# Kernel optimization log

Measured on AMD Instinct MI355X. Metric: run time of the kernel, lower is better.

The kernel has to match this reference:

```python
import jax, jax.numpy as jnp
import numpy as np

HEADS = 4
ALPHA = 0.2  # leaky relu negative slope


def setup_inputs() -> dict:
    key = jax.random.key(0)
    ks = jax.random.split(key, 8)
    N, Fin, Fout = 4096, 512, 256
    return {
        "h": jax.random.normal(ks[0], (N, Fin), dtype=jnp.float32),
        "adj": jax.random.randint(ks[1], (N, N), 0, 2, dtype=jnp.int32),
        "W": jax.random.normal(ks[2], (Fin, Fout), dtype=jnp.float32) * (Fin ** -0.5),
        "Wl_w": jax.random.normal(ks[3], (Fout, Fout), dtype=jnp.float32) * (Fout ** -0.5),
        "Wl_b": jax.random.normal(ks[4], (Fout,), dtype=jnp.float32) * 0.02,
        "Wqkv_w": jax.random.normal(ks[5], (3 * Fout, Fout), dtype=jnp.float32) * (Fout ** -0.5),
        "Wqkv_b": jax.random.normal(ks[6], (3 * Fout,), dtype=jnp.float32) * 0.02,
        "a": jax.random.normal(ks[7], (2 * Fout, 1), dtype=jnp.float32) * (Fout ** -0.5),
    }


def reference(h, adj, W, Wl_w, Wl_b, Wqkv_w, Wqkv_b, a):
    N = h.shape[0]
    Fout = W.shape[1]
    d = Fout // HEADS
    scale = Fout ** -0.5  # note: original scales by out_features^-0.5, not head_dim

    Wh = h @ W                      # [N, Fout]
    Wh = Wh @ Wl_w.T + Wl_b         # to_linear

    qkv = Wh @ Wqkv_w.T + Wqkv_b    # [N, 3*Fout]
    q, k, v = jnp.split(qkv, 3, axis=-1)
    to_heads = lambda t: t.reshape(N, HEADS, d).transpose(1, 0, 2)  # [H, N, d]
    q, k, v = to_heads(q), to_heads(k), to_heads(v)

    dots = jax.nn.softmax(jnp.einsum('hid,hjd->hij', q, k) * scale, axis=-1)  # [H,N,N]
    Wh0 = jnp.einsum('hij,hjd->hid', dots, v)            # [H, N, d]
    Wh0 = Wh0.transpose(1, 0, 2).reshape(N, Fout)        # i (h d)
    Wh0 = jax.nn.softmax(Wh0, axis=-1)

    # GAT score decomposed: e_ij = leakyrelu(Wh_i . a1 + Wh_j . a2)
    a1 = a[:Fout, 0]
    a2 = a[Fout:, 0]
    e = jax.nn.leaky_relu((Wh @ a1)[:, None] + (Wh @ a2)[None, :], negative_slope=ALPHA)

    dsum = dots.sum(axis=0)                              # [N, N]
    neg = jnp.float32(-9e15)
    attention = jnp.where(adj > 0, e + dsum, neg)
    attention = jax.nn.softmax(attention, axis=1)
    # dropout p=0.0 / eval mode -> identity

    h_prime = attention @ Wh + Wh0
    return jax.nn.elu(h_prime)  # concat=True
```

## Files before the change

kernel.cpp:

```cpp
#include <hip/hip_runtime.h>

typedef float  f32x4 __attribute__((ext_vector_type(4)));
typedef short  s16x8 __attribute__((ext_vector_type(8)));
typedef unsigned short u16x8 __attribute__((ext_vector_type(8)));

#define NROWS 4096
#define ALPHA_LR 0.2f
#define SCALE 0.0625f

static __device__ __forceinline__ unsigned short bf16_rne(float x) {
    unsigned u = __float_as_uint(x);
    u += 0x7fffu + ((u >> 16) & 1u);
    return (unsigned short)(u >> 16);
}
static __device__ __forceinline__ unsigned short bf16_trunc(float x) {
    return (unsigned short)(__float_as_uint(x) >> 16);
}
static __device__ __forceinline__ float bf2f(unsigned short h) {
    return __uint_as_float(((unsigned)h) << 16);
}
static __device__ __forceinline__ float bflo(unsigned u) { return __uint_as_float(u << 16); }
static __device__ __forceinline__ float bfhi(unsigned u) { return __uint_as_float(u & 0xffff0000u); }
static __device__ __forceinline__ float wmax16(float v) {
#pragma unroll
    for (int o = 8; o; o >>= 1) v = fmaxf(v, __shfl_xor(v, o, 16));
    return v;
}
static __device__ __forceinline__ float wsum16(float v) {
#pragma unroll
    for (int o = 8; o; o >>= 1) v += __shfl_xor(v, o, 16);
    return v;
}

__global__ __launch_bounds__(256) void wprep(
    const float* __restrict__ W, const float* __restrict__ Wq,
    unsigned short* __restrict__ Whi, unsigned short* __restrict__ Wlo,
    unsigned short* __restrict__ Qhi, unsigned short* __restrict__ Qlo)
{
    int i = blockIdx.x * 256 + threadIdx.x;
    if (i < 131072) {
        float v = W[i];
        unsigned short hh = bf16_trunc(v);
        Whi[i] = hh; Wlo[i] = bf16_rne(v - bf2f(hh));
    }
    if (i < 196608) {
        float v = Wq[i];
        unsigned short hh = bf16_trunc(v);
        Qhi[i] = hh; Qlo[i] = bf16_rne(v - bf2f(hh));
    }
}

template <int EPI, bool BIAS>
__global__ __launch_bounds__(256) void gemm_mfma(
    const float* __restrict__ A,
    const unsigned short* __restrict__ Bhi, const unsigned short* __restrict__ Blo,
    const float* __restrict__ bias,
    float* __restrict__ C, unsigned short* __restrict__ o0,
    unsigned short* __restrict__ o1, unsigned short* __restrict__ o2,
    int M, int Nn, int K)
{
    __shared__ unsigned short Ah[64][40];
    __shared__ unsigned short Al[64][40];
    __shared__ unsigned short Bh[64][40];
    __shared__ unsigned short Bl[64][40];

    const int tid = threadIdx.x;
    const int w = tid >> 6;
    const int ln = tid & 63;
    const int l15 = ln & 15;
    const int lhi = ln >> 4;
    const int bm = blockIdx.y * 64;
    const int bn = blockIdx.x * 64;
    const int sm = tid >> 2;
    const int sk = (tid & 3) * 8;

    f32x4 acc[4];
#pragma unroll
    for (int cf = 0; cf < 4; ++cf) acc[cf] = (f32x4){0.f, 0.f, 0.f, 0.f};

    const float* arow = &A[(size_t)(bm + sm) * K];
    const unsigned short* bhrow = &Bhi[(size_t)(bn + sm) * K];
    const unsigned short* blrow = &Blo[(size_t)(bn + sm) * K];

    float4 a0r = *(const float4*)(arow + sk);
    float4 a1r = *(const float4*)(arow + sk + 4);
    uint4 bhr = *(const uint4*)(bhrow + sk);
    uint4 blr = *(const uint4*)(blrow + sk);

    for (int k0 = 0; k0 < K; k0 += 32) {
        float vv[8] = {a0r.x, a0r.y, a0r.z, a0r.w, a1r.x, a1r.y, a1r.z, a1r.w};
        unsigned hp[4], lp[4];
#pragma unroll
        for (int q = 0; q < 4; ++q) {
            unsigned short h0 = bf16_trunc(vv[q * 2]);
            unsigned short h1 = bf16_trunc(vv[q * 2 + 1]);
            unsigned short l0 = bf16_rne(vv[q * 2] - bf2f(h0));
            unsigned short l1 = bf16_rne(vv[q * 2 + 1] - bf2f(h1));
            hp[q] = (unsigned)h0 | ((unsigned)h1 << 16);
            lp[q] = (unsigned)l0 | ((unsigned)l1 << 16);
        }
        __syncthreads();
        *(uint4*)&Ah[sm][sk] = make_uint4(hp[0], hp[1], hp[2], hp[3]);
        *(uint4*)&Al[sm][sk] = make_uint4(lp[0], lp[1], lp[2], lp[3]);
        *(uint4*)&Bh[sm][sk] = bhr;
        *(uint4*)&Bl[sm][sk] = blr;
        const int kn = (k0 + 32 < K) ? k0 + 32 : 0;
        a0r = *(const float4*)(arow + kn + sk);
        a1r = *(const float4*)(arow + kn + sk + 4);
        bhr = *(const uint4*)(bhrow + kn + sk);
        blr = *(const uint4*)(blrow + kn + sk);
        __syncthreads();
        s16x8 ah = *(const s16x8*)&Ah[w * 16 + l15][lhi * 8];
        s16x8 al2 = *(const s16x8*)&Al[w * 16 + l15][lhi * 8];
        __builtin_amdgcn_s_setprio(1);
#pragma unroll
        for (int cf = 0; cf < 4; ++cf) {
            s16x8 bh = *(const s16x8*)&Bh[cf * 16 + l15][lhi * 8];
            s16x8 bl = *(const s16x8*)&Bl[cf * 16 + l15][lhi * 8];
            acc[cf] = __builtin_amdgcn_mfma_f32_16x16x32_bf16(ah, bh, acc[cf], 0, 0, 0);
            acc[cf] = __builtin_amdgcn_mfma_f32_16x16x32_bf16(ah, bl, acc[cf], 0, 0, 0);
            acc[cf] = __builtin_amdgcn_mfma_f32_16x16x32_bf16(al2, bh, acc[cf], 0, 0, 0);
        }
        __builtin_amdgcn_s_setprio(0);
    }

#pragma unroll
    for (int cf = 0; cf < 4; ++cf) {
        const int col = bn + cf * 16 + l15;
        float bv = BIAS ? bias[col] : 0.0f;
#pragma unroll
        for (int r = 0; r < 4; ++r) {
            const int row = bm + w * 16 + lhi * 4 + r;
            float v = acc[cf][r] + bv;
            if (EPI == 1) {
                C[(size_t)row * Nn + col] = v;
                o0[(size_t)col * NROWS + row] = bf16_rne(v);
            } else if (EPI == 2) {
                if (col < 256)      o0[(size_t)row * 256 + col] = bf16_rne(v);
                else if (col < 512) o1[(size_t)row * 256 + (col - 256)] = bf16_rne(v);
                else                o2[(size_t)(col - 512) * NROWS + row] = bf16_rne(v);
            } else {
                unsigned short hh = bf16_trunc(v);
                o0[(size_t)row * Nn + col] = hh;
                o1[(size_t)row * Nn + col] = bf16_rne(v - bf2f(hh));
            }
        }
    }
}

__global__ __launch_bounds__(256) void compute_p(
    const float* __restrict__ Wh, const float* __restrict__ a,
    float* __restrict__ p1, float* __restrict__ p2)
{
    const int row = blockIdx.x * 16 + (threadIdx.x >> 4);
    const int c = threadIdx.x & 15;
    float s1 = 0.f, s2 = 0.f;
    for (int f = c; f < 256; f += 16) {
        float w = Wh[(size_t)row * 256 + f];
        s1 += w * a[f];
        s2 += w * a[256 + f];
    }
    s1 = wsum16(s1);
    s2 = wsum16(s2);
    if (c == 0) { p1[row] = s1; p2[row] = s2; }
}

__global__ __launch_bounds__(256) void p2max_kernel(
    const float* __restrict__ p2, float* __restrict__ p2m)
{
    __shared__ float red[4];
    const int tid = threadIdx.x;
    float v = -3.0e38f;
#pragma unroll
    for (int k = 0; k < 16; ++k) v = fmaxf(v, p2[tid + k * 256]);
#pragma unroll
    for (int o = 32; o; o >>= 1) v = fmaxf(v, __shfl_xor(v, o, 64));
    if ((tid & 63) == 0) red[tid >> 6] = v;
    __syncthreads();
    if (tid == 0) p2m[0] = fmaxf(fmaxf(red[0], red[1]), fmaxf(red[2], red[3]));
}

__global__ __launch_bounds__(256) void norms1(
    const unsigned short* __restrict__ qh, const unsigned short* __restrict__ kh,
    float* __restrict__ qn2, float* __restrict__ knp)
{
    __shared__ float kn[16][4];
    const int tid = threadIdx.x;
    const int r16 = tid >> 4;
    const int c = tid & 15;
    const int i = blockIdx.x * 16 + r16;
#pragma unroll
    for (int h = 0; h < 4; ++h) {
        float sq = 0.f, sk = 0.f;
#pragma unroll
        for (int d = 0; d < 4; ++d) {
            float qv = bf2f(qh[(size_t)i * 256 + h * 64 + c + d * 16]);
            float kv = bf2f(kh[(size_t)i * 256 + h * 64 + c + d * 16]);
            sq += qv * qv; sk += kv * kv;
        }
        sq = wsum16(sq); sk = wsum16(sk);
        if (c == 0) { qn2[i * 4 + h] = sq; kn[r16][h] = sk; }
    }
    __syncthreads();
    if (tid < 4) {
        float m = 0.f;
#pragma unroll
        for (int r = 0; r < 16; ++r) m = fmaxf(m, kn[r][tid]);
        knp[blockIdx.x * 4 + tid] = m;
    }
}

__global__ __launch_bounds__(256) void norms2(
    const float* __restrict__ qn2, const float* __restrict__ knp,
    float* __restrict__ Mb)
{
    __shared__ float red[4][4];
    __shared__ float kmax[4];
    const int tid = threadIdx.x;
    float v[4];
#pragma unroll
    for (int h = 0; h < 4; ++h) v[h] = knp[tid * 4 + h];
#pragma unroll
    for (int h = 0; h < 4; ++h)
#pragma unroll
        for (int o = 32; o; o >>= 1) v[h] = fmaxf(v[h], __shfl_xor(v[h], o, 64));
    if ((tid & 63) == 0) {
#pragma unroll
        for (int h = 0; h < 4; ++h) red[tid >> 6][h] = v[h];
    }
    __syncthreads();
    if (tid < 4)
        kmax[tid] = fmaxf(fmaxf(red[0][tid], red[1][tid]), fmaxf(red[2][tid], red[3][tid]));
    __syncthreads();
    const int i = blockIdx.x * 256 + tid;
#pragma unroll
    for (int h = 0; h < 4; ++h)
        Mb[i * 4 + h] = sqrtf(qn2[i * 4 + h] * kmax[h]) * SCALE;
}

__global__ __launch_bounds__(256) void zsum_kernel(
    const unsigned short* __restrict__ qh_g, const unsigned short* __restrict__ kh_g,
    const float* __restrict__ Mb, float* __restrict__ zpart)
{
    const int tid = threadIdx.x;
    const int h = tid >> 6;
    const int ln = tid & 63;
    const int l15 = ln & 15;
    const int lhi = ln >> 4;
    const int rt = blockIdx.x & 255;
    const int ch = blockIdx.x >> 8;
    const int i0 = rt * 16;

    s16x8 qA[2];
#pragma unroll
    for (int ks = 0; ks < 2; ++ks)
        qA[ks] = *(const s16x8*)(qh_g + (size_t)(i0 + l15) * 256 + h * 64 + ks * 32 + lhi * 8);
    float M[4];
#pragma unroll
    for (int r = 0; r < 4; ++r) M[r] = Mb[(i0 + lhi * 4 + r) * 4 + h];

    float z[4] = {0.f, 0.f, 0.f, 0.f};
    s16x8 kfc[2][2];
#pragma unroll
    for (int nt = 0; nt < 2; ++nt)
#pragma unroll
        for (int ks = 0; ks < 2; ++ks)
            kfc[nt][ks] = *(const s16x8*)(kh_g + (size_t)(ch * 1024 + nt * 16 + l15) * 256 +
                                          h * 64 + ks * 32 + lhi * 8);

    for (int tt = 0; tt < 32; ++tt) {
        const int jn = ch * 1024 + ((tt + 1) & 31) * 32;
        f32x4 acc[2] = {{0.f,0.f,0.f,0.f},{0.f,0.f,0.f,0.f}};
        __builtin_amdgcn_s_setprio(1);
#pragma unroll
        for (int ks = 0; ks < 2; ++ks)
#pragma unroll
            for (int nt = 0; nt < 2; ++nt)
                acc[nt] = __builtin_amdgcn_mfma_f32_16x16x32_bf16(qA[ks], kfc[nt][ks], acc[nt], 0, 0, 0);
        __builtin_amdgcn_s_setprio(0);
#pragma unroll
        for (int nt = 0; nt < 2; ++nt)
#pragma unroll
            for (int ks = 0; ks < 2; ++ks)
                kfc[nt][ks] = *(const s16x8*)(kh_g + (size_t)(jn + nt * 16 + l15) * 256 +
                                              h * 64 + ks * 32 + lhi * 8);
#pragma unroll
        for (int r = 0; r < 4; ++r)
            z[r] += __expf(acc[0][r] * SCALE - M[r]) + __expf(acc[1][r] * SCALE - M[r]);
    }
#pragma unroll
    for (int r = 0; r < 4; ++r) {
        float zz = wsum16(z[r]);
        if (l15 == 0)
            zpart[(((size_t)(i0 + lhi * 4 + r) * 4 + h) * 4) + ch] = zz;
    }
}

__global__ __launch_bounds__(256) void pvds_kernel(
    const unsigned short* __restrict__ qh_g, const unsigned short* __restrict__ kh_g,
    const unsigned short* __restrict__ vth_g,
    const float* __restrict__ Mb, const float* __restrict__ zpart,
    unsigned short* __restrict__ dsum_g, unsigned short* __restrict__ pacc_o)
{
    enum { D0 = 0, D1 = 5120, MIZ = 10240, SMEMSZ = 10752 };
    __shared__ __align__(16) char smem[SMEMSZ];

    const int tid = threadIdx.x;
    const int h = tid >> 6;
    const int ln = tid & 63;
    const int l15 = ln & 15;
    const int lhi = ln >> 4;
    const int rt = blockIdx.x & 255;
    const int ch = blockIdx.x >> 8;
    const int i0 = rt * 16;
    const int srow = tid >> 4;
    const int sc2 = (tid & 15) * 2;

    if (tid < 64) {
        int hh = tid >> 4, row = tid & 15;
        float M = Mb[(i0 + row) * 4 + hh];
        const float* zb = zpart + ((size_t)(i0 + row) * 4 + hh) * 4;
        float z = ((zb[0] + zb[1]) + zb[2]) + zb[3];
        float* fl = (float*)(smem + MIZ);
        fl[(hh * 16 + row) * 2] = M;
        fl[(hh * 16 + row) * 2 + 1] = 1.0f / z;
    }

    s16x8 qA[2];
#pragma unroll
    for (int ks = 0; ks < 2; ++ks)
        qA[ks] = *(const s16x8*)(qh_g + (size_t)(i0 + l15) * 256 + h * 64 + ks * 32 + lhi * 8);
    __syncthreads();

    float m_f[4], iz_f[4];
#pragma unroll
    for (int r = 0; r < 4; ++r) {
        m_f[r]  = ((float*)(smem + MIZ))[(h * 16 + lhi * 4 + r) * 2];
        iz_f[r] = ((float*)(smem + MIZ))[(h * 16 + lhi * 4 + r) * 2 + 1];
    }

    s16x8 kfc[2][2], vfc[2];
#pragma unroll
    for (int nt = 0; nt < 2; ++nt)
#pragma unroll
        for (int ks = 0; ks < 2; ++ks)
            kfc[nt][ks] = *(const s16x8*)(kh_g + (size_t)(ch * 1024 + nt * 16 + l15) * 256 +
                                          h * 64 + ks * 32 + lhi * 8);
#pragma unroll
    for (int nt = 0; nt < 2; ++nt)
        vfc[nt] = *(const s16x8*)(vth_g + (size_t)(h * 64 + nt * 16 + l15) * 4096 +
                                  ch * 1024 + lhi * 8);

    f32x4 pacc[2] = {{0.f,0.f,0.f,0.f},{0.f,0.f,0.f,0.f}};

    for (int tt = 0; tt < 32; ++tt) {
        const int j0 = ch * 1024 + tt * 32;
        const int jn = ch * 1024 + ((tt + 1) & 31) * 32;
        const int buf = (tt & 1) ? D1 : D0;

        f32x4 acc[2] = {{0.f,0.f,0.f,0.f},{0.f,0.f,0.f,0.f}};
        __builtin_amdgcn_s_setprio(1);
#pragma unroll
        for (int ks = 0; ks < 2; ++ks)
#pragma unroll
            for (int nt = 0; nt < 2; ++nt)
                acc[nt] = __builtin_amdgcn_mfma_f32_16x16x32_bf16(qA[ks], kfc[nt][ks], acc[nt], 0, 0, 0);
        __builtin_amdgcn_s_setprio(0);
#pragma unroll
        for (int nt = 0; nt < 2; ++nt)
#pragma unroll
            for (int ks = 0; ks < 2; ++ks)
                kfc[nt][ks] = *(const s16x8*)(kh_g + (size_t)(jn + nt * 16 + l15) * 256 +
                                              h * 64 + ks * 32 + lhi * 8);
#pragma unroll
        for (int nt = 0; nt < 2; ++nt)
#pragma unroll
            for (int r = 0; r < 4; ++r) {
                float d = __expf(acc[nt][r] * SCALE - m_f[r]) * iz_f[r];
                int row = lhi * 4 + r;
                *(unsigned short*)(smem + buf + h * 1280 + row * 80 + (nt * 16 + l15) * 2) = bf16_rne(d);
            }
        __syncthreads();

        {
            s16x8 dA = *(const s16x8*)(smem + buf + h * 1280 + l15 * 80 + lhi * 16);
            __builtin_amdgcn_s_setprio(1);
            pacc[0] = __builtin_amdgcn_mfma_f32_16x16x32_bf16(dA, vfc[0], pacc[0], 0, 0, 0);
            pacc[1] = __builtin_amdgcn_mfma_f32_16x16x32_bf16(dA, vfc[1], pacc[1], 0, 0, 0);
            __builtin_amdgcn_s_setprio(0);
        }
#pragma unroll
        for (int nt = 0; nt < 2; ++nt)
            vfc[nt] = *(const s16x8*)(vth_g + (size_t)(h * 64 + nt * 16 + l15) * 4096 + jn + lhi * 8);

        {
            float ds0 = 0.f, ds1 = 0.f;
#pragma unroll
            for (int hh = 0; hh < 4; ++hh) {
                unsigned u = *(const unsigned*)(smem + buf + hh * 1280 + srow * 80 + sc2 * 2);
                ds0 += bflo(u); ds1 += bfhi(u);
            }
            unsigned pk = (unsigned)bf16_rne(ds0) | ((unsigned)bf16_rne(ds1) << 16);
            *(unsigned*)(dsum_g + (size_t)(i0 + srow) * 4096 + j0 + sc2) = pk;
        }
    }

    const size_t pbase = (size_t)(rt * 4 + ch) * 4096;
#pragma unroll
    for (int nt = 0; nt < 2; ++nt)
#pragma unroll
        for (int r = 0; r < 4; ++r)
            pacc_o[pbase + (lhi * 4 + r) * 256 + h * 64 + nt * 16 + l15] = bf16_rne(pacc[nt][r]);
}

__global__ __launch_bounds__(256) void outer_kernel(
    const unsigned short* __restrict__ wht_g, const unsigned short* __restrict__ dsum_g,
    const float* __restrict__ p1g, const float* __restrict__ p2g,
    const float* __restrict__ p2m, const int* __restrict__ adj,
    unsigned short* __restrict__ wacc_o, float* __restrict__ Lp_o)
{
    enum { PT0 = 0, PT1 = 2304, SMEMSZ = 4608 };
    __shared__ __align__(16) char smem[SMEMSZ];

    const int tid = threadIdx.x;
    const int w = tid >> 6;
    const int ln = tid & 63;
    const int l15 = ln & 15;
    const int lhi = ln >> 4;
    const int rt = blockIdx.x & 255;
    const int ch = blockIdx.x >> 8;
    const int i0 = rt * 16;
    const int jbase = ch * 1024;
    const int srow = tid >> 4;
    const int sc4 = (tid & 15) * 4;

    const float p1v = p1g[i0 + srow];
    float Mfix;
    {
        float s = p1v + p2m[0];
        Mfix = (s > 0.f ? s : ALPHA_LR * s) + 4.0f;
    }

    int4   adjc = *(const int4*)(adj + (size_t)(i0 + srow) * 4096 + jbase + sc4);
    ushort4 dsc = *(const ushort4*)(dsum_g + (size_t)(i0 + srow) * 4096 + jbase + sc4);
    float4 p2c  = *(const float4*)(p2g + jbase + sc4);
    s16x8 wfc[4][2];
#pragma unroll
    for (int nt = 0; nt < 4; ++nt)
#pragma unroll
        for (int ks = 0; ks < 2; ++ks)
            wfc[nt][ks] = *(const s16x8*)(wht_g + (size_t)(w * 64 + nt * 16 + l15) * 4096 +
                                          jbase + ks * 32 + lhi * 8);

    f32x4 acc[4];
#pragma unroll
    for (int nt = 0; nt < 4; ++nt) acc[nt] = (f32x4){0.f, 0.f, 0.f, 0.f};
    float Lacc = 0.0f;

    for (int t = 0; t < 16; ++t) {
        const int jn = jbase + ((t + 1) & 15) * 64;
        const int buf = (t & 1) ? PT1 : PT0;

        {
            float pr[4];
            float dsv[4] = {bf2f(dsc.x), bf2f(dsc.y), bf2f(dsc.z), bf2f(dsc.w)};
            float p2v[4] = {p2c.x, p2c.y, p2c.z, p2c.w};
            int   av[4]  = {adjc.x, adjc.y, adjc.z, adjc.w};
#pragma unroll
            for (int k = 0; k < 4; ++k) {
                float e = p1v + p2v[k];
                e = e > 0.f ? e : ALPHA_LR * e;
                pr[k] = (av[k] > 0) ? __expf(e + dsv[k] - Mfix) : 0.f;
                Lacc += pr[k];
            }
            ushort4 pk;
            pk.x = bf16_rne(pr[0]); pk.y = bf16_rne(pr[1]);
            pk.z = bf16_rne(pr[2]); pk.w = bf16_rne(pr[3]);
            *(ushort4*)(smem + buf + srow * 144 + sc4 * 2) = pk;
        }
        adjc = *(const int4*)(adj + (size_t)(i0 + srow) * 4096 + jn + sc4);
        dsc  = *(const ushort4*)(dsum_g + (size_t)(i0 + srow) * 4096 + jn + sc4);
        p2c  = *(const float4*)(p2g + jn + sc4);
        __syncthreads();

        {
            s16x8 pa0 = *(const s16x8*)(smem + buf + l15 * 144 + lhi * 16);
            s16x8 pa1 = *(const s16x8*)(smem + buf + l15 * 144 + 64 + lhi * 16);
            __builtin_amdgcn_s_setprio(1);
#pragma unroll
            for (int nt = 0; nt < 4; ++nt) {
                acc[nt] = __builtin_amdgcn_mfma_f32_16x16x32_bf16(pa0, wfc[nt][0], acc[nt], 0, 0, 0);
                acc[nt] = __builtin_amdgcn_mfma_f32_16x16x32_bf16(pa1, wfc[nt][1], acc[nt], 0, 0, 0);
            }
            __builtin_amdgcn_s_setprio(0);
        }
#pragma unroll
        for (int nt = 0; nt < 4; ++nt)
#pragma unroll
            for (int ks = 0; ks < 2; ++ks)
                wfc[nt][ks] = *(const s16x8*)(wht_g + (size_t)(w * 64 + nt * 16 + l15) * 4096 +
                                              jn + ks * 32 + lhi * 8);
    }

    Lacc = wsum16(Lacc);
    if ((tid & 15) == 0) Lp_o[(size_t)(rt * 4 + ch) * 16 + srow] = Lacc;

    const size_t wbase = (size_t)(rt * 4 + ch) * 4096;
#pragma unroll
    for (int nt = 0; nt < 4; ++nt)
#pragma unroll
        for (int r = 0; r < 4; ++r)
            wacc_o[wbase + (lhi * 4 + r) * 256 + w * 64 + nt * 16 + l15] = bf16_rne(acc[nt][r]);
}

__global__ __launch_bounds__(256) void merge_kernel(
    const unsigned short* __restrict__ pacc_b, const unsigned short* __restrict__ wacc_b,
    const float* __restrict__ Lp, float* __restrict__ out)
{
    const int rt = blockIdx.x;
    const int tid = threadIdx.x;
    const int row = tid >> 4;
    const int cg = tid & 15;

    float L = 0.f;
#pragma unroll
    for (int c = 0; c < 4; ++c) L += Lp[(size_t)(rt * 4 + c) * 16 + row];
    const float invL = 1.0f / fmaxf(L, 1e-30f);

    float p[16], wv[16];
#pragma unroll
    for (int k = 0; k < 16; ++k) { p[k] = 0.f; wv[k] = 0.f; }
#pragma unroll
    for (int c = 0; c < 4; ++c) {
        const size_t b = (size_t)(rt * 4 + c) * 4096 + row * 256 + cg * 16;
        u16x8 pa0 = *(const u16x8*)(pacc_b + b);
        u16x8 pa1 = *(const u16x8*)(pacc_b + b + 8);
        u16x8 wa0 = *(const u16x8*)(wacc_b + b);
        u16x8 wa1 = *(const u16x8*)(wacc_b + b + 8);
#pragma unroll
        for (int k = 0; k < 8; ++k) {
            p[k] += bf2f(pa0[k]);  p[k + 8] += bf2f(pa1[k]);
            wv[k] += bf2f(wa0[k]); wv[k + 8] += bf2f(wa1[k]);
        }
    }

    float mx = -3.0e38f;
#pragma unroll
    for (int k = 0; k < 16; ++k) mx = fmaxf(mx, p[k]);
    mx = wmax16(mx);
    float sm = 0.f;
#pragma unroll
    for (int k = 0; k < 16; ++k) { p[k] = __expf(p[k] - mx); sm += p[k]; }
    sm = wsum16(sm);
    const float inv = 1.0f / sm;

    float* orow = out + ((size_t)(rt * 16 + row)) * 256 + cg * 16;
#pragma unroll
    for (int k4 = 0; k4 < 4; ++k4) {
        float4 o;
        float v;
        v = wv[k4*4+0] * invL + p[k4*4+0] * inv; o.x = v > 0.f ? v : __expf(v) - 1.f;
        v = wv[k4*4+1] * invL + p[k4*4+1] * inv; o.y = v > 0.f ? v : __expf(v) - 1.f;
        v = wv[k4*4+2] * invL + p[k4*4+2] * inv; o.z = v > 0.f ? v : __expf(v) - 1.f;
        v = wv[k4*4+3] * invL + p[k4*4+3] * inv; o.w = v > 0.f ? v : __expf(v) - 1.f;
        *(float4*)(orow + k4 * 4) = o;
    }
}

extern "C" void kernel_launch(void* const* d_in, const int* in_sizes, int n_in,
                              void* d_out, int out_size, void* d_ws, size_t ws_size,
                              hipStream_t stream)
{
    const float* h      = (const float*)d_in[0];
    const int*   adj    = (const int*)d_in[1];
    const float* W      = (const float*)d_in[2];
    const float* Wl_w   = (const float*)d_in[3];
    const float* Wl_b   = (const float*)d_in[4];
    const float* Wqkv_w = (const float*)d_in[5];
    const float* Wqkv_b = (const float*)d_in[6];
    const float* a      = (const float*)d_in[7];
    float* out = (float*)d_out;

    char* wsb = (char*)d_ws;
    unsigned short* qh     = (unsigned short*)(wsb + 0);
    unsigned short* kh     = (unsigned short*)(wsb + 2097152);
    unsigned short* vth    = (unsigned short*)(wsb + 4194304);
    unsigned short* wht    = (unsigned short*)(wsb + 6291456);
    unsigned short* dsum_b = (unsigned short*)(wsb + 8388608);
    unsigned short* pacc_b = (unsigned short*)(wsb + 41943040);
    unsigned short* wacc_b = (unsigned short*)(wsb + 50331648);
    float*          Whb    = (float*)(wsb + 50331648);
    unsigned short* Whi    = (unsigned short*)(wsb + 58720256);
    unsigned short* Wlo    = Whi + 131072;
    unsigned short* Qhi    = Wlo + 131072;
    unsigned short* Qlo    = Qhi + 196608;
    unsigned short* WcThi  = Qlo + 196608;
    unsigned short* WcTlo  = WcThi + 131072;
    float*          p1b    = (float*)(wsb + 60555264);
    float*          p2b    = (float*)(wsb + 60571648);
    float*          p2m    = (float*)(wsb + 60588032);
    float*          qn2    = (float*)(wsb + 60592128);
    float*          knp    = (float*)(wsb + 60657664);
    float*          Mb     = (float*)(wsb + 60661760);
    float*          zpart  = (float*)(wsb + 60727296);
    float*          Lp     = (float*)(wsb + 60989440);

    dim3 blk(256);
    wprep<<<dim3(768), blk, 0, stream>>>(W, Wqkv_w, Whi, Wlo, Qhi, Qlo);
    gemm_mfma<3, false><<<dim3(8, 4), blk, 0, stream>>>(
        Wl_w, Whi, Wlo, nullptr, nullptr, WcThi, WcTlo, nullptr, 256, 512, 256);
    gemm_mfma<1, true><<<dim3(4, 64), blk, 0, stream>>>(
        h, WcThi, WcTlo, Wl_b, Whb, wht, nullptr, nullptr, 4096, 256, 512);
    gemm_mfma<2, true><<<dim3(12, 64), blk, 0, stream>>>(
        Whb, Qhi, Qlo, Wqkv_b, nullptr, qh, kh, vth, 4096, 768, 256);
    compute_p<<<dim3(256), blk, 0, stream>>>(Whb, a, p1b, p2b);
    p2max_kernel<<<dim3(1), blk, 0, stream>>>(p2b, p2m);
    norms1<<<dim3(256), blk, 0, stream>>>(qh, kh, qn2, knp);
    norms2<<<dim3(16), blk, 0, stream>>>(qn2, knp, Mb);
    zsum_kernel<<<dim3(1024), blk, 0, stream>>>(qh, kh, Mb, zpart);
    pvds_kernel<<<dim3(1024), blk, 0, stream>>>(qh, kh, vth, Mb, zpart, dsum_b, pacc_b);
    outer_kernel<<<dim3(1024), blk, 0, stream>>>(wht, dsum_b, p1b, p2b, p2m, adj, wacc_b, Lp);
    merge_kernel<<<dim3(256), blk, 0, stream>>>(pacc_b, wacc_b, Lp, out);
}
```

Before: 286.0 us.

## Split key range into eight chunks and reduce partials with float atomics

Halves the per-block j-range in the zsum, pvds and outer kernels, so each launches twice as many blocks. Partial results for P·V, adjacency·Wh and the softmax denominators are now accumulated with float atomicAdd into zeroed fp32 buffers, replacing per-chunk bf16 partial buffers that merge_kernel had to sum. The outer kernel also builds its MFMA A-fragment directly in registers, dropping the LDS staging and the barrier. In exchange it adds memsets, atomic contention on shared output rows, and nondeterministic summation order.

```diff
diff --git a/kernel.cpp b/kernel.cpp
--- a/kernel.cpp
+++ b/kernel.cpp
@@ -7,6 +7,8 @@
 #define NROWS 4096
 #define ALPHA_LR 0.2f
 #define SCALE 0.0625f
+#define NCHUNK 8
+#define CHJ 512
 
 static __device__ __forceinline__ unsigned short bf16_rne(float x) {
     unsigned u = __float_as_uint(x);
@@ -250,6 +252,7 @@
     const int rt = blockIdx.x & 255;
     const int ch = blockIdx.x >> 8;
     const int i0 = rt * 16;
+    const int jb = ch * CHJ;
 
     s16x8 qA[2];
 #pragma unroll
@@ -265,11 +268,11 @@
     for (int nt = 0; nt < 2; ++nt)
 #pragma unroll
         for (int ks = 0; ks < 2; ++ks)
-            kfc[nt][ks] = *(const s16x8*)(kh_g + (size_t)(ch * 1024 + nt * 16 + l15) * 256 +
+            kfc[nt][ks] = *(const s16x8*)(kh_g + (size_t)(jb + nt * 16 + l15) * 256 +
                                           h * 64 + ks * 32 + lhi * 8);
 
-    for (int tt = 0; tt < 32; ++tt) {
-        const int jn = ch * 1024 + ((tt + 1) & 31) * 32;
+    for (int tt = 0; tt < 16; ++tt) {
+        const int jn = jb + ((tt + 1) & 15) * 32;
         f32x4 acc[2] = {{0.f,0.f,0.f,0.f},{0.f,0.f,0.f,0.f}};
         __builtin_amdgcn_s_setprio(1);
 #pragma unroll
@@ -286,13 +289,13 @@
                                               h * 64 + ks * 32 + lhi * 8);
 #pragma unroll
         for (int r = 0; r < 4; ++r)
-            z[r] += __expf(acc[0][r] * SCALE - M[r]) + __expf(acc[1][r] * SCALE - M[r]);
+            z[r] += __expf(fmaf(acc[0][r], SCALE, -M[r])) + __expf(fmaf(acc[1][r], SCALE, -M[r]));
     }
 #pragma unroll
     for (int r = 0; r < 4; ++r) {
         float zz = wsum16(z[r]);
         if (l15 == 0)
-            zpart[(((size_t)(i0 + lhi * 4 + r) * 4 + h) * 4) + ch] = zz;
+            zpart[(((size_t)(i0 + lhi * 4 + r) * 4 + h) * NCHUNK) + ch] = zz;
     }
 }
 
@@ -300,7 +303,7 @@
     const unsigned short* __restrict__ qh_g, const unsigned short* __restrict__ kh_g,
     const unsigned short* __restrict__ vth_g,
     const float* __restrict__ Mb, const float* __restrict__ zpart,
-    unsigned short* __restrict__ dsum_g, unsigned short* __restrict__ pacc_o)
+    unsigned short* __restrict__ dsum_g, float* __restrict__ pacc_g)
 {
     enum { D0 = 0, D1 = 5120, MIZ = 10240, SMEMSZ = 10752 };
     __shared__ __align__(16) char smem[SMEMSZ];
@@ -313,16 +316,18 @@
     const int rt = blockIdx.x & 255;
     const int ch = blockIdx.x >> 8;
     const int i0 = rt * 16;
+    const int jb = ch * CHJ;
     const int srow = tid >> 4;
     const int sc2 = (tid & 15) * 2;
 
     if (tid < 64) {
         int hh = tid >> 4, row = tid & 15;
-        float M = Mb[(i0 + row) * 4 + hh];
-        const float* zb = zpart + ((size_t)(i0 + row) * 4 + hh) * 4;
-        float z = ((zb[0] + zb[1]) + zb[2]) + zb[3];
+        const float* zb = zpart + ((size_t)(i0 + row) * 4 + hh) * NCHUNK;
+        float z = 0.f;
+#pragma unroll
+        for (int c = 0; c < NCHUNK; ++c) z += zb[c];
         float* fl = (float*)(smem + MIZ);
-        fl[(hh * 16 + row) * 2] = M;
+        fl[(hh * 16 + row) * 2] = Mb[(i0 + row) * 4 + hh];
         fl[(hh * 16 + row) * 2 + 1] = 1.0f / z;
     }
 
@@ -335,27 +340,29 @@
     float m_f[4], iz_f[4];
 #pragma unroll
     for (int r = 0; r < 4; ++r) {
-        m_f[r]  = ((float*)(smem + MIZ))[(h * 16 + lhi * 4 + r) * 2];
-        iz_f[r] = ((float*)(smem + MIZ))[(h * 16 + lhi * 4 + r) * 2 + 1];
-    }
-
-    s16x8 kfc[2][2], vfc[2];
+        m_f[r]  = ((const float*)(smem + MIZ))[(h * 16 + lhi * 4 + r) * 2];
+        iz_f[r] = ((const float*)(smem + MIZ))[(h * 16 + lhi * 4 + r) * 2 + 1];
+    }
+
+    s16x8 kfc[2][2], vfc[4];
 #pragma unroll
     for (int nt = 0; nt < 2; ++nt)
 #pragma unroll
         for (int ks = 0; ks < 2; ++ks)
-            kfc[nt][ks] = *(const s16x8*)(kh_g + (size_t)(ch * 1024 + nt * 16 + l15) * 256 +
+            kfc[nt][ks] = *(const s16x8*)(kh_g + (size_t)(jb + nt * 16 + l15) * 256 +
                                           h * 64 + ks * 32 + lhi * 8);
 #pragma unroll
-    for (int nt = 0; nt < 2; ++nt)
-        vfc[nt] = *(const s16x8*)(vth_g + (size_t)(h * 64 + nt * 16 + l15) * 4096 +
-                                  ch * 1024 + lhi * 8);
-
-    f32x4 pacc[2] = {{0.f,0.f,0.f,0.f},{0.f,0.f,0.f,0.f}};
-
-    for (int tt = 0; tt < 32; ++tt) {
-        const int j0 = ch * 1024 + tt * 32;
-        const int jn = ch * 1024 + ((tt + 1) & 31) * 32;
+    for (int nt2 = 0; nt2 < 4; ++nt2)
+        vfc[nt2] = *(const s16x8*)(vth_g + (size_t)(h * 64 + nt2 * 16 + l15) * 4096 +
+                                   jb + lhi * 8);
+
+    f32x4 pacc[4];
+#pragma unroll
+    for (int nt2 = 0; nt2 < 4; ++nt2) pacc[nt2] = (f32x4){0.f, 0.f, 0.f, 0.f};
+
+    for (int tt = 0; tt < 16; ++tt) {
+        const int j0 = jb + tt * 32;
+        const int jn = jb + ((tt + 1) & 15) * 32;
         const int buf = (tt & 1) ? D1 : D0;
 
         f32x4 acc[2] = {{0.f,0.f,0.f,0.f},{0.f,0.f,0.f,0.f}};
@@ -376,7 +383,7 @@
         for (int nt = 0; nt < 2; ++nt)
 #pragma unroll
             for (int r = 0; r < 4; ++r) {
-                float d = __expf(acc[nt][r] * SCALE - m_f[r]) * iz_f[r];
+                float d = __expf(fmaf(acc[nt][r], SCALE, -m_f[r])) * iz_f[r];
                 int row = lhi * 4 + r;
                 *(unsigned short*)(smem + buf + h * 1280 + row * 80 + (nt * 16 + l15) * 2) = bf16_rne(d);
             }
@@ -385,13 +392,15 @@
         {
             s16x8 dA = *(const s16x8*)(smem + buf + h * 1280 + l15 * 80 + lhi * 16);
             __builtin_amdgcn_s_setprio(1);
-            pacc[0] = __builtin_amdgcn_mfma_f32_16x16x32_bf16(dA, vfc[0], pacc[0], 0, 0, 0);
-            pacc[1] = __builtin_amdgcn_mfma_f32_16x16x32_bf16(dA, vfc[1], pacc[1], 0, 0, 0);
+#pragma unroll
+            for (int nt2 = 0; nt2 < 4; ++nt2)
+                pacc[nt2] = __builtin_amdgcn_mfma_f32_16x16x32_bf16(dA, vfc[nt2], pacc[nt2], 0, 0, 0);
             __builtin_amdgcn_s_setprio(0);
         }
 #pragma unroll
-        for (int nt = 0; nt < 2; ++nt)
-            vfc[nt] = *(const s16x8*)(vth_g + (size_t)(h * 64 + nt * 16 + l15) * 4096 + jn + lhi * 8);
+        for (int nt2 = 0; nt2 < 4; ++nt2)
+            vfc[nt2] = *(const s16x8*)(vth_g + (size_t)(h * 64 + nt2 * 16 + l15) * 4096 +
+                                       jn + lhi * 8);
 
         {
             float ds0 = 0.f, ds1 = 0.f;
@@ -405,23 +414,20 @@
         }
     }
 
-    const size_t pbase = (size_t)(rt * 4 + ch) * 4096;
-#pragma unroll
-    for (int nt = 0; nt < 2; ++nt)
+#pragma unroll
+    for (int nt2 = 0; nt2 < 4; ++nt2)
 #pragma unroll
         for (int r = 0; r < 4; ++r)
-            pacc_o[pbase + (lhi * 4 + r) * 256 + h * 64 + nt * 16 + l15] = bf16_rne(pacc[nt][r]);
+            atomicAdd(&pacc_g[(size_t)(i0 + lhi * 4 + r) * 256 + h * 64 + nt2 * 16 + l15],
+                      pacc[nt2][r]);
 }
 
 __global__ __launch_bounds__(256) void outer_kernel(
     const unsigned short* __restrict__ wht_g, const unsigned short* __restrict__ dsum_g,
     const float* __restrict__ p1g, const float* __restrict__ p2g,
     const float* __restrict__ p2m, const int* __restrict__ adj,
-    unsigned short* __restrict__ wacc_o, float* __restrict__ Lp_o)
-{
-    enum { PT0 = 0, PT1 = 2304, SMEMSZ = 4608 };
-    __shared__ __align__(16) char smem[SMEMSZ];
-
+    float* __restrict__ wacc_g, float* __restrict__ Lp_g)
+{
     const int tid = threadIdx.x;
     const int w = tid >> 6;
     const int ln = tid & 63;
@@ -430,27 +436,30 @@
     const int rt = blockIdx.x & 255;
     const int ch = blockIdx.x >> 8;
     const int i0 = rt * 16;
-    const int jbase = ch * 1024;
-    const int srow = tid >> 4;
-    const int sc4 = (tid & 15) * 4;
-
-    const float p1v = p1g[i0 + srow];
+    const int jb = ch * CHJ;
+    const int i = i0 + l15;
+
+    const float p1v = p1g[i];
     float Mfix;
     {
         float s = p1v + p2m[0];
         Mfix = (s > 0.f ? s : ALPHA_LR * s) + 4.0f;
     }
 
-    int4   adjc = *(const int4*)(adj + (size_t)(i0 + srow) * 4096 + jbase + sc4);
-    ushort4 dsc = *(const ushort4*)(dsum_g + (size_t)(i0 + srow) * 4096 + jbase + sc4);
-    float4 p2c  = *(const float4*)(p2g + jbase + sc4);
-    s16x8 wfc[4][2];
+    const int* adjB = adj + (size_t)i * 4096 + lhi * 8;
+    const unsigned short* dsB = dsum_g + (size_t)i * 4096 + lhi * 8;
+    const float* p2B = p2g + lhi * 8;
+    const unsigned short* whB = wht_g + lhi * 8;
+
+    int4 a0 = *(const int4*)(adjB + jb);
+    int4 a1 = *(const int4*)(adjB + jb + 4);
+    u16x8 ds = *(const u16x8*)(dsB + jb);
+    float4 q0 = *(const float4*)(p2B + jb);
+    float4 q1 = *(const float4*)(p2B + jb + 4);
+    s16x8 wf[4];
 #pragma unroll
     for (int nt = 0; nt < 4; ++nt)
-#pragma unroll
-        for (int ks = 0; ks < 2; ++ks)
-            wfc[nt][ks] = *(const s16x8*)(wht_g + (size_t)(w * 64 + nt * 16 + l15) * 4096 +
-                                          jbase + ks * 32 + lhi * 8);
+        wf[nt] = *(const s16x8*)(whB + (size_t)(w * 64 + nt * 16 + l15) * 4096 + jb);
 
     f32x4 acc[4];
 #pragma unroll
@@ -458,90 +467,74 @@
     float Lacc = 0.0f;
 
     for (int t = 0; t < 16; ++t) {
-        const int jn = jbase + ((t + 1) & 15) * 64;
-        const int buf = (t & 1) ? PT1 : PT0;
-
+        const int jn = jb + ((t + 1) & 15) * 32;
+
+        float pr[8];
         {
-            float pr[4];
-            float dsv[4] = {bf2f(dsc.x), bf2f(dsc.y), bf2f(dsc.z), bf2f(dsc.w)};
-            float p2v[4] = {p2c.x, p2c.y, p2c.z, p2c.w};
-            int   av[4]  = {adjc.x, adjc.y, adjc.z, adjc.w};
-#pragma unroll
-            for (int k = 0; k < 4; ++k) {
-                float e = p1v + p2v[k];
+            int am[8] = {a0.x, a0.y, a0.z, a0.w, a1.x, a1.y, a1.z, a1.w};
+            float pv[8] = {q0.x, q0.y, q0.z, q0.w, q1.x, q1.y, q1.z, q1.w};
+#pragma unroll
+            for (int k = 0; k < 8; ++k) {
+                float e = p1v + pv[k];
                 e = e > 0.f ? e : ALPHA_LR * e;
-                pr[k] = (av[k] > 0) ? __expf(e + dsv[k] - Mfix) : 0.f;
+                float arg = e + bf2f((unsigned short)ds[k]) - Mfix;
+                pr[k] = (am[k] > 0) ? __expf(arg) : 0.f;
                 Lacc += pr[k];
             }
-            ushort4 pk;
-            pk.x = bf16_rne(pr[0]); pk.y = bf16_rne(pr[1]);
-            pk.z = bf16_rne(pr[2]); pk.w = bf16_rne(pr[3]);
-            *(ushort4*)(smem + buf + srow * 144 + sc4 * 2) = pk;
         }
-        adjc = *(const int4*)(adj + (size_t)(i0 + srow) * 4096 + jn + sc4);
-        dsc  = *(const ushort4*)(dsum_g + (size_t)(i0 + srow) * 4096 + jn + sc4);
-        p2c  = *(const float4*)(p2g + jn + sc4);
-        __syncthreads();
-
-        {
-            s16x8 pa0 = *(const s16x8*)(smem + buf + l15 * 144 + lhi * 16);
-            s16x8 pa1 = *(const s16x8*)(smem + buf + l15 * 144 + 64 + lhi * 16);
-            __builtin_amdgcn_s_setprio(1);
-#pragma unroll
-            for (int nt = 0; nt < 4; ++nt) {
-                acc[nt] = __builtin_amdgcn_mfma_f32_16x16x32_bf16(pa0, wfc[nt][0], acc[nt], 0, 0, 0);
-                acc[nt] = __builtin_amdgcn_mfma_f32_16x16x32_bf16(pa1, wfc[nt][1], acc[nt], 0, 0, 0);
-            }
-            __builtin_amdgcn_s_setprio(0);
-        }
+        a0 = *(const int4*)(adjB + jn);
+        a1 = *(const int4*)(adjB + jn + 4);
+        ds = *(const u16x8*)(dsB + jn);
+        q0 = *(const float4*)(p2B + jn);
+        q1 = *(const float4*)(p2B + jn + 4);
+
+        s16x8 pA;
+#pragma unroll
+        for (int k = 0; k < 8; ++k) pA[k] = (short)bf16_rne(pr[k]);
+
+        __builtin_amdgcn_s_setprio(1);
 #pragma unroll
         for (int nt = 0; nt < 4; ++nt)
-#pragma unroll
-            for (int ks = 0; ks < 2; ++ks)
-                wfc[nt][ks] = *(const s16x8*)(wht_g + (size_t)(w * 64 + nt * 16 + l15) * 4096 +
-                                              jn + ks * 32 + lhi * 8);
-    }
-
-    Lacc = wsum16(Lacc);
-    if ((tid & 15) == 0) Lp_o[(size_t)(rt * 4 + ch) * 16 + srow] = Lacc;
-
-    const size_t wbase = (size_t)(rt * 4 + ch) * 4096;
+            acc[nt] = __builtin_amdgcn_mfma_f32_16x16x32_bf16(pA, wf[nt], acc[nt], 0, 0, 0);
+        __builtin_amdgcn_s_setprio(0);
+
+#pragma unroll
+        for (int nt = 0; nt < 4; ++nt)
+            wf[nt] = *(const s16x8*)(whB + (size_t)(w * 64 + nt * 16 + l15) * 4096 + jn);
+    }
+
+    Lacc += __shfl_xor(Lacc, 16);
+    Lacc += __shfl_xor(Lacc, 32);
+    if (w == 0 && ln < 16) atomicAdd(&Lp_g[i], Lacc);
+
 #pragma unroll
     for (int nt = 0; nt < 4; ++nt)
 #pragma unroll
         for (int r = 0; r < 4; ++r)
-            wacc_o[wbase + (lhi * 4 + r) * 256 + w * 64 + nt * 16 + l15] = bf16_rne(acc[nt][r]);
+            atomicAdd(&wacc_g[(size_t)(i0 + lhi * 4 + r) * 256 + w * 64 + nt * 16 + l15],
+                      acc[nt][r]);
 }
 
 __global__ __launch_bounds__(256) void merge_kernel(
-    const unsigned short* __restrict__ pacc_b, const unsigned short* __restrict__ wacc_b,
+    const float* __restrict__ pacc_g, const float* __restrict__ wacc_g,
     const float* __restrict__ Lp, float* __restrict__ out)
 {
     const int rt = blockIdx.x;
     const int tid = threadIdx.x;
     const int row = tid >> 4;
     const int cg = tid & 15;
-
-    float L = 0.f;
-#pragma unroll
-    for (int c = 0; c < 4; ++c) L += Lp[(size_t)(rt * 4 + c) * 16 + row];
-    const float invL = 1.0f / fmaxf(L, 1e-30f);
+    const int i = rt * 16 + row;
+
+    const float invL = 1.0f / fmaxf(Lp[i], 1e-30f);
 
     float p[16], wv[16];
-#pragma unroll
-    for (int k = 0; k < 16; ++k) { p[k] = 0.f; wv[k] = 0.f; }
-#pragma unroll
-    for (int c = 0; c < 4; ++c) {
-        const size_t b = (size_t)(rt * 4 + c) * 4096 + row * 256 + cg * 16;
-        u16x8 pa0 = *(const u16x8*)(pacc_b + b);
-        u16x8 pa1 = *(const u16x8*)(pacc_b + b + 8);
-        u16x8 wa0 = *(const u16x8*)(wacc_b + b);
-        u16x8 wa1 = *(const u16x8*)(wacc_b + b + 8);
-#pragma unroll
-        for (int k = 0; k < 8; ++k) {
-            p[k] += bf2f(pa0[k]);  p[k + 8] += bf2f(pa1[k]);
-            wv[k] += bf2f(wa0[k]); wv[k + 8] += bf2f(wa1[k]);
-        }
+    const size_t b = (size_t)i * 256 + cg * 16;
+#pragma unroll
+    for (int k4 = 0; k4 < 4; ++k4) {
+        float4 pv = *(const float4*)(pacc_g + b + k4 * 4);
+        float4 wvv = *(const float4*)(wacc_g + b + k4 * 4);
+        p[k4*4+0] = pv.x; p[k4*4+1] = pv.y; p[k4*4+2] = pv.z; p[k4*4+3] = pv.w;
+        wv[k4*4+0] = wvv.x; wv[k4*4+1] = wvv.y; wv[k4*4+2] = wvv.z; wv[k4*4+3] = wvv.w;
     }
 
     float mx = -3.0e38f;
@@ -554,7 +547,7 @@
     sm = wsum16(sm);
     const float inv = 1.0f / sm;
 
-    float* orow = out + ((size_t)(rt * 16 + row)) * 256 + cg * 16;
+    float* orow = out + (size_t)i * 256 + cg * 16;
 #pragma unroll
     for (int k4 = 0; k4 < 4; ++k4) {
         float4 o;
@@ -587,23 +580,27 @@
     unsigned short* vth    = (unsigned short*)(wsb + 4194304);
     unsigned short* wht    = (unsigned short*)(wsb + 6291456);
     unsigned short* dsum_b = (unsigned short*)(wsb + 8388608);
-    unsigned short* pacc_b = (unsigned short*)(wsb + 41943040);
-    unsigned short* wacc_b = (unsigned short*)(wsb + 50331648);
-    float*          Whb    = (float*)(wsb + 50331648);
-    unsigned short* Whi    = (unsigned short*)(wsb + 58720256);
+    float*          pacc_f = (float*)(wsb + 41943040);
+    float*          wacc_f = (float*)(wsb + 46137344);
+    float*          p1b    = (float*)(wsb + 50331648);
+    float*          p2b    = (float*)(wsb + 50348032);
+    float*          p2m    = (float*)(wsb + 50364416);
+    float*          qn2    = (float*)(wsb + 50368512);
+    float*          knp    = (float*)(wsb + 50434048);
+    float*          Mb     = (float*)(wsb + 50438144);
+    float*          zpart  = (float*)(wsb + 50503680);
+    float*          Lp     = (float*)(wsb + 51027968);
+    float*          Whb    = (float*)(wsb + 8388608);
+    unsigned short* Whi    = (unsigned short*)(wsb + 12582912);
     unsigned short* Wlo    = Whi + 131072;
     unsigned short* Qhi    = Wlo + 131072;
     unsigned short* Qlo    = Qhi + 196608;
     unsigned short* WcThi  = Qlo + 196608;
     unsigned short* WcTlo  = WcThi + 131072;
-    float*          p1b    = (float*)(wsb + 60555264);
-    float*          p2b    = (float*)(wsb + 60571648);
-    float*          p2m    = (float*)(wsb + 60588032);
-    float*          qn2    = (float*)(wsb + 60592128);
-    float*          knp    = (float*)(wsb + 60657664);
-    float*          Mb     = (float*)(wsb + 60661760);
-    float*          zpart  = (float*)(wsb + 60727296);
-    float*          Lp     = (float*)(wsb + 60989440);
+
+    hipMemsetAsync(pacc_f, 0, 4194304, stream);
+    hipMemsetAsync(wacc_f, 0, 4194304, stream);
+    hipMemsetAsync(Lp, 0, 16384, stream);
 
     dim3 blk(256);
     wprep<<<dim3(768), blk, 0, stream>>>(W, Wqkv_w, Whi, Wlo, Qhi, Qlo);
@@ -617,8 +614,8 @@
     p2max_kernel<<<dim3(1), blk, 0, stream>>>(p2b, p2m);
     norms1<<<dim3(256), blk, 0, stream>>>(qh, kh, qn2, knp);
     norms2<<<dim3(16), blk, 0, stream>>>(qn2, knp, Mb);
-    zsum_kernel<<<dim3(1024), blk, 0, stream>>>(qh, kh, Mb, zpart);
-    pvds_kernel<<<dim3(1024), blk, 0, stream>>>(qh, kh, vth, Mb, zpart, dsum_b, pacc_b);
-    outer_kernel<<<dim3(1024), blk, 0, stream>>>(wht, dsum_b, p1b, p2b, p2m, adj, wacc_b, Lp);
-    merge_kernel<<<dim3(256), blk, 0, stream>>>(pacc_b, wacc_b, Lp, out);
-}
+    zsum_kernel<<<dim3(2048), blk, 0, stream>>>(qh, kh, Mb, zpart);
+    pvds_kernel<<<dim3(2048), blk, 0, stream>>>(qh, kh, vth, Mb, zpart, dsum_b, pacc_f);
+    outer_kernel<<<dim3(2048), blk, 0, stream>>>(wht, dsum_b, p1b, p2b, p2m, adj, wacc_f, Lp);
+    merge_kernel<<<dim3(256), blk, 0, stream>>>(pacc_f, wacc_f, Lp, out);
+}
```

After: 377.1 us. +31.8%, slower.
